# Performance work log

Hardware: AMD Instinct MI355X
Metric: run time of the kernel (lower is better)

Reference implementation:

```python
import jax, jax.numpy as jnp
import numpy as np

N_BLADES = 8
D_BLADE = 128
D_FFN = 512
LN_EPS = 1e-5


def _build_cayley_signs():
    """Cl(3,0) Cayley table: blades indexed by bitmask over {e1,e2,e3}.
    signs[i, j, k] = s where blade_i * blade_j = s * blade_k (Euclidean metric)."""
    def reorder_sign(a, b):
        a >>= 1
        total = 0
        while a:
            total += bin(a & b).count('1')
            a >>= 1
        return 1.0 if total % 2 == 0 else -1.0
    signs = np.zeros((8, 8, 8), dtype=np.float32)
    for i in range(8):
        for j in range(8):
            signs[i, j, i ^ j] = reorder_sign(i, j)
    return jnp.asarray(signs)


def setup_inputs() -> dict:
    key = jax.random.key(0)
    k_x, k_g, k_u, k_d = jax.random.split(key, 4)
    B, T = 4, 4096
    x = jax.random.normal(k_x, (B, T, N_BLADES, D_BLADE), dtype=jnp.float32)
    return {
        'x': x,
        'interaction_weights': jnp.full((N_BLADES, N_BLADES), 0.1, dtype=jnp.float32),
        'geo_gate': jnp.asarray(0.5, dtype=jnp.float32),
        'ln_w': jnp.ones((D_BLADE,), dtype=jnp.float32),
        'ln_b': jnp.zeros((D_BLADE,), dtype=jnp.float32),
        'w_gate': jax.random.normal(k_g, (D_FFN, D_BLADE), dtype=jnp.float32) * 0.02,
        'w_up': jax.random.normal(k_u, (D_FFN, D_BLADE), dtype=jnp.float32) * 0.02,
        'w_down': jax.random.normal(k_d, (D_BLADE, D_FFN), dtype=jnp.float32) * 0.02,
        'cayley_signs': _build_cayley_signs(),
    }


def reference(x, interaction_weights, geo_gate, ln_w, ln_b, w_gate, w_up, w_down, cayley_signs):
    # --- full geometric self-product via Cayley table ---
    w = jax.nn.sigmoid(interaction_weights)              # (i, j)
    signed = cayley_signs * w[:, :, None]                # (i, j, k): fold weights into sign tensor
    # result[b,t,k,d] = sum_ij signed[i,j,k] * x[b,t,i,d] * x[b,t,j,d]
    geo = jnp.einsum('btid,btjd,ijk->btkd', x, x, signed)
    # --- residual gate between geometric product and input ---
    gate = jax.nn.sigmoid(geo_gate)
    mixed = gate * geo + (1.0 - gate) * x                # (B, T, N, D)
    # --- per-blade LayerNorm over d_blade ---
    mu = jnp.mean(mixed, axis=-1, keepdims=True)
    var = jnp.mean(jnp.square(mixed - mu), axis=-1, keepdims=True)
    normed = (mixed - mu) * jax.lax.rsqrt(var + LN_EPS) * ln_w + ln_b
    # --- SwiGLU FFN (no biases) ---
    g = jnp.einsum('btnd,fd->btnf', normed, w_gate)
    u = jnp.einsum('btnd,fd->btnf', normed, w_up)
    h = jax.nn.silu(g) * u
    out = jnp.einsum('btnf,df->btnd', h, w_down)
    return x + out
```

## Files before the change

kernel.cpp:

```cpp
#include <hip/hip_runtime.h>
#include <hip/hip_bf16.h>

typedef unsigned short ushort_t;
typedef __bf16 bf16_t;
typedef bf16_t bf16x8 __attribute__((ext_vector_type(8)));
typedef unsigned short u16x8v __attribute__((ext_vector_type(8)));
typedef float f32x4 __attribute__((ext_vector_type(4)));
typedef unsigned uint32x2 __attribute__((ext_vector_type(2)));
typedef unsigned uint32x4 __attribute__((ext_vector_type(4)));

#define D 128
#define NB 8
#define DFFN 512
#define LN_EPS 1e-5f

#define BARRIER_LGKM() asm volatile("s_waitcnt lgkmcnt(0)\n\ts_barrier" ::: "memory")
#define BARRIER_VM()   asm volatile("s_waitcnt vmcnt(0) lgkmcnt(0)\n\ts_barrier" ::: "memory")

__device__ __forceinline__ ushort_t bf16_rne(float f) {
  union { float f; unsigned u; } c; c.f = f;
  unsigned u = c.u;
  unsigned r = (u + 0x7FFFu + ((u >> 16) & 1u)) >> 16;
  return (ushort_t)r;
}

__device__ __forceinline__ unsigned cvt_pk_bf16(float lo, float hi) {
  unsigned r;
  asm("v_cvt_pk_bf16_f32 %0, %1, %2" : "=v"(r) : "v"(lo), "v"(hi));
  return r;
}

__device__ __forceinline__ bf16x8 loadfrag_bf(const ushort_t* p) {
  u16x8v v = *(const u16x8v*)p;
  return __builtin_bit_cast(bf16x8, v);
}

__device__ __forceinline__ bf16x8 load8_cvt(const float* p) {
  f32x4 a = *(const f32x4*)p;
  f32x4 b = *(const f32x4*)(p + 4);
  u16x8v r;
  r[0] = bf16_rne(a[0]); r[1] = bf16_rne(a[1]);
  r[2] = bf16_rne(a[2]); r[3] = bf16_rne(a[3]);
  r[4] = bf16_rne(b[0]); r[5] = bf16_rne(b[1]);
  r[6] = bf16_rne(b[2]); r[7] = bf16_rne(b[3]);
  return __builtin_bit_cast(bf16x8, r);
}

__device__ __forceinline__ f32x4 mfma16(bf16x8 a, bf16x8 b, f32x4 c) {
  return __builtin_amdgcn_mfma_f32_16x16x32_bf16(a, b, c, 0, 0, 0);
}

__device__ __forceinline__ float readlane_f(float v, int lane) {
  return __builtin_bit_cast(float, __builtin_amdgcn_readlane(__builtin_bit_cast(int, v), lane));
}

__device__ __forceinline__ float fast_rcp(float x) {
  return __builtin_amdgcn_rcpf(x);
}

typedef const __attribute__((address_space(1))) void gv_t;
typedef __attribute__((address_space(3))) void lv_t;
__device__ __forceinline__ void gload_lds16(const void* g, void* l) {
  __builtin_amdgcn_global_load_lds((gv_t*)g, (lv_t*)l, 16, 0, 0);
}

__global__ void cvt_weights(const float* __restrict__ wg,
                            const float* __restrict__ wu,
                            const float* __restrict__ wd,
                            ushort_t* __restrict__ o) {
  int i = blockIdx.x * 256 + threadIdx.x;
  const int n1 = DFFN * D;
  float v;
  if (i < n1)            v = wg[i];
  else if (i < 2 * n1)   v = wu[i - n1];
  else                   v = wd[i - 2 * n1];
  o[i] = bf16_rne(v);
}

__global__ __launch_bounds__(256)
void geo_ln(const float* __restrict__ x,
            const float* __restrict__ iw,
            const float* __restrict__ geo_gate,
            const float* __restrict__ ln_w,
            const float* __restrict__ ln_b,
            const float* __restrict__ cayley,
            ushort_t* __restrict__ Aout) {
  const int tid = threadIdx.x;
  const int w = tid >> 6;
  const int l = tid & 63;
  const int g = l >> 4;
  const int q = l & 15;

  float sgv;
  {
    int i_l = l >> 3, j_l = l & 7;
    float s = cayley[(i_l * 8 + j_l) * 8 + (i_l ^ j_l)];
    sgv = s / (1.0f + __expf(-iw[i_l * 8 + j_l]));
  }
  float cd[8], cp[28];
#pragma unroll
  for (int i = 0; i < 8; ++i) cd[i] = readlane_f(sgv, i * 8 + i);
  {
    int p = 0;
#pragma unroll
    for (int i = 0; i < 8; ++i)
#pragma unroll
      for (int j = i + 1; j < 8; ++j) { cp[p] = readlane_f(sgv, i * 8 + j) + readlane_f(sgv, j * 8 + i); ++p; }
  }
  const float gate = 1.0f / (1.0f + __expf(-geo_gate[0]));
  const float ogate = 1.0f - gate;

  const f32x4 lw0 = *(const f32x4*)(ln_w + q * 8);
  const f32x4 lw1 = *(const f32x4*)(ln_w + q * 8 + 4);
  const f32x4 lb0 = *(const f32x4*)(ln_b + q * 8);
  const f32x4 lb1 = *(const f32x4*)(ln_b + q * 8 + 4);

  const long tok = (long)blockIdx.x * 16 + w * 4 + g;
  const float* xp = x + tok * (NB * D) + q * 8;

  f32x4 xa[8], xb[8];
#pragma unroll
  for (int i = 0; i < 8; ++i) { xa[i] = *(const f32x4*)(xp + i * D); xb[i] = *(const f32x4*)(xp + i * D + 4); }

  f32x4 ga[8], gb[8];
#pragma unroll
  for (int k = 0; k < 8; ++k) { ga[k] = 0.f; gb[k] = 0.f; }
#pragma unroll
  for (int i = 0; i < 8; ++i) {
    ga[0] += cd[i] * (xa[i] * xa[i]);
    gb[0] += cd[i] * (xb[i] * xb[i]);
  }
  {
    int p = 0;
#pragma unroll
    for (int i = 0; i < 8; ++i)
#pragma unroll
      for (int j = i + 1; j < 8; ++j) {
        int k = i ^ j;
        ga[k] += cp[p] * (xa[i] * xa[j]);
        gb[k] += cp[p] * (xb[i] * xb[j]);
        ++p;
      }
  }

  ushort_t* Arow0 = Aout + tok * (8 * D);
#pragma unroll
  for (int k = 0; k < 8; ++k) {
    f32x4 m0 = gate * ga[k] + ogate * xa[k];
    f32x4 m1 = gate * gb[k] + ogate * xb[k];
    float s1 = (m0[0] + m0[1]) + (m0[2] + m0[3]) + (m1[0] + m1[1]) + (m1[2] + m1[3]);
    float s2 = m0[0]*m0[0] + m0[1]*m0[1] + m0[2]*m0[2] + m0[3]*m0[3]
             + m1[0]*m1[0] + m1[1]*m1[1] + m1[2]*m1[2] + m1[3]*m1[3];
#pragma unroll
    for (int off = 8; off; off >>= 1) {
      s1 += __shfl_xor(s1, off, 64);
      s2 += __shfl_xor(s2, off, 64);
    }
    float mu = s1 * (1.0f / 128.0f);
    float rs = rsqrtf(s2 * (1.0f / 128.0f) - mu * mu + LN_EPS);
    float nb2 = -mu * rs;
    f32x4 n0, n1;
#pragma unroll
    for (int e = 0; e < 4; ++e) {
      n0[e] = (m0[e] * rs + nb2) * lw0[e] + lb0[e];
      n1[e] = (m1[e] * rs + nb2) * lw1[e] + lb1[e];
    }
    uint32x4 pk;
    pk[0] = cvt_pk_bf16(n0[0], n0[1]);
    pk[1] = cvt_pk_bf16(n0[2], n0[3]);
    pk[2] = cvt_pk_bf16(n1[0], n1[1]);
    pk[3] = cvt_pk_bf16(n1[2], n1[3]);
    *(uint32x4*)(Arow0 + k * D + ((q ^ k) * 8)) = pk;
  }
}

__global__ __launch_bounds__(256, 3)
void ffn_mfma(const ushort_t* __restrict__ Abf,
              const float* __restrict__ x,
              const ushort_t* __restrict__ wg_bf,
              const ushort_t* __restrict__ wu_bf,
              const ushort_t* __restrict__ wd_bf,
              float* __restrict__ out) {
  __shared__ ushort_t A[64 * 128];
  __shared__ ushort_t Hb[2][64 * 64];

  const int tid = threadIdx.x;
  const int w = tid >> 6;
  const int l = tid & 63;
  const int lg = l >> 4;
  const int ln16 = l & 15;

  const long row0 = (long)blockIdx.x * 64;

  {
    const ushort_t* src = Abf + row0 * D;
#pragma unroll
    for (int i = 0; i < 4; ++i) {
      int seg = w * 4 + i;
      gload_lds16(src + seg * 512 + l * 8, &A[seg * 512]);
    }
  }

  bf16x8 bg[4], bu[4], bd[2][2];
  {
    const int frow = w * 16 + ln16;
#pragma unroll
    for (int ks = 0; ks < 4; ++ks) {
      bg[ks] = loadfrag_bf(wg_bf + frow * D + ks * 32 + lg * 8);
      bu[ks] = loadfrag_bf(wu_bf + frow * D + ks * 32 + lg * 8);
    }
#pragma unroll
    for (int nt = 0; nt < 2; ++nt) {
      int dcol = w * 32 + nt * 16 + ln16;
#pragma unroll
      for (int k2 = 0; k2 < 2; ++k2)
        bd[nt][k2] = loadfrag_bf(wd_bf + dcol * DFFN + k2 * 32 + lg * 8);
    }
  }

  BARRIER_VM();

  f32x4 oacc[4][2];
#pragma unroll
  for (int mt = 0; mt < 4; ++mt)
#pragma unroll
    for (int nt = 0; nt < 2; ++nt)
#pragma unroll
      for (int r = 0; r < 4; ++r) oacc[mt][nt][r] = 0.f;

#pragma unroll
  for (int ch = 0; ch < 8; ++ch) {
    ushort_t* Hc = &Hb[ch & 1][0];

#pragma unroll
    for (int mt = 0; mt < 4; ++mt) {
      const int row = mt * 16 + ln16;
      f32x4 gacc = 0.f, uacc = 0.f;
      __builtin_amdgcn_s_setprio(1);
#pragma unroll
      for (int ks = 0; ks < 4; ++ks) {
        int unit = (ks * 4 + lg) ^ (row & 7);
        bf16x8 a = *(const bf16x8*)&A[row * 128 + unit * 8];
        gacc = mfma16(bg[ks], a, gacc);
        uacc = mfma16(bu[ks], a, uacc);
      }
      __builtin_amdgcn_s_setprio(0);
      float h[4];
#pragma unroll
      for (int r = 0; r < 4; ++r) {
        float gv = gacc[r];
        h[r] = gv * fast_rcp(1.0f + __expf(-gv)) * uacc[r];
      }
      uint32x2 pk;
      pk[0] = cvt_pk_bf16(h[0], h[1]);
      pk[1] = cvt_pk_bf16(h[2], h[3]);
      int u = (w * 2 + (lg >> 1)) ^ (row & 7);
      *(uint32x2*)((char*)Hc + row * 128 + u * 16 + (lg & 1) * 8) = pk;
    }

    if (ch < 7) {
      const int frow = (ch + 1) * 64 + w * 16 + ln16;
#pragma unroll
      for (int ks = 0; ks < 4; ++ks) {
        bg[ks] = loadfrag_bf(wg_bf + frow * D + ks * 32 + lg * 8);
        bu[ks] = loadfrag_bf(wu_bf + frow * D + ks * 32 + lg * 8);
      }
    }

    BARRIER_LGKM();

    __builtin_amdgcn_s_setprio(1);
#pragma unroll
    for (int mt = 0; mt < 4; ++mt) {
      const int m = mt * 16 + ln16;
#pragma unroll
      for (int k2 = 0; k2 < 2; ++k2) {
        int u = (k2 * 4 + lg) ^ (m & 7);
        bf16x8 hf = *(const bf16x8*)((const char*)Hc + m * 128 + u * 16);
        oacc[mt][0] = mfma16(hf, bd[0][k2], oacc[mt][0]);
        oacc[mt][1] = mfma16(hf, bd[1][k2], oacc[mt][1]);
      }
    }
    __builtin_amdgcn_s_setprio(0);

    if (ch < 7) {
#pragma unroll
      for (int nt = 0; nt < 2; ++nt) {
        int dcol = w * 32 + nt * 16 + ln16;
#pragma unroll
        for (int k2 = 0; k2 < 2; ++k2)
          bd[nt][k2] = loadfrag_bf(wd_bf + dcol * DFFN + (ch + 1) * 64 + k2 * 32 + lg * 8);
      }
    }
  }

#pragma unroll
  for (int mt = 0; mt < 4; ++mt) {
#pragma unroll
    for (int r = 0; r < 4; ++r) {
      long rowg = row0 + mt * 16 + lg * 4 + r;
      const float* xp = x + rowg * D;
      float* op = out + rowg * D;
#pragma unroll
      for (int nt = 0; nt < 2; ++nt) {
        int d = w * 32 + nt * 16 + ln16;
        op[d] = xp[d] + oacc[mt][nt][r];
      }
    }
  }
}

template <bool WS_BF16>
__global__ __launch_bounds__(256, 2)
void fused_geo_ffn(const float* __restrict__ x,
                   const float* __restrict__ iw,
                   const float* __restrict__ geo_gate,
                   const float* __restrict__ ln_w,
                   const float* __restrict__ ln_b,
                   const float* __restrict__ w_gate_f,
                   const float* __restrict__ w_up_f,
                   const float* __restrict__ w_down_f,
                   const float* __restrict__ cayley,
                   const ushort_t* __restrict__ wg_bf,
                   const ushort_t* __restrict__ wu_bf,
                   const ushort_t* __restrict__ wd_bf,
                   float* __restrict__ out) {
  __shared__ float sg[64];
  __shared__ ushort_t A_lds[128 * 128];
  __shared__ ushort_t H_lds[128 * 64];

  const int tid = threadIdx.x;
  const int w = tid >> 6;
  const int l = tid & 63;
  const int lg = l >> 4;
  const int ln16 = l & 15;
  const int kbase = lg * 8;

  if (tid < 64) {
    int i = tid >> 3, j = tid & 7;
    float s = cayley[(i * 8 + j) * 8 + (i ^ j)];
    sg[tid] = s / (1.0f + __expf(-iw[i * 8 + j]));
  }
  __syncthreads();
  float sgr[64];
#pragma unroll
  for (int t = 0; t < 64; ++t) sgr[t] = sg[t];

  const float gate = 1.0f / (1.0f + __expf(-geo_gate[0]));
  const float2 lw = *(const float2*)(ln_w + 2 * l);
  const float2 lb = *(const float2*)(ln_b + 2 * l);
  const long tok0 = (long)blockIdx.x * 16;

  for (int tt = 0; tt < 4; ++tt) {
    int ltok = w * 4 + tt;
    const float* xp = x + (tok0 + ltok) * (long)(NB * D);
    float2 xv[8];
#pragma unroll
    for (int i = 0; i < 8; ++i) xv[i] = *(const float2*)(xp + i * D + 2 * l);
#pragma unroll
    for (int k = 0; k < 8; ++k) {
      float2 g; g.x = 0.f; g.y = 0.f;
#pragma unroll
      for (int i = 0; i < 8; ++i) {
        float s = sgr[i * 8 + (i ^ k)];
        g.x += s * xv[i].x * xv[i ^ k].x;
        g.y += s * xv[i].y * xv[i ^ k].y;
      }
      float2 m;
      m.x = gate * g.x + (1.0f - gate) * xv[k].x;
      m.y = gate * g.y + (1.0f - gate) * xv[k].y;
      float s1 = m.x + m.y;
      float s2 = m.x * m.x + m.y * m.y;
#pragma unroll
      for (int off = 32; off; off >>= 1) {
        s1 += __shfl_xor(s1, off, 64);
        s2 += __shfl_xor(s2, off, 64);
      }
      float mu = s1 * (1.0f / 128.0f);
      float rs = rsqrtf(s2 * (1.0f / 128.0f) - mu * mu + LN_EPS);
      float nx = (m.x - mu) * rs * lw.x + lb.x;
      float ny = (m.y - mu) * rs * lw.y + lb.y;
      int row = ltok * 8 + k;
      int colb = (4 * l) ^ ((row & 7) << 4);
      *(unsigned*)((char*)A_lds + row * 256 + colb) = cvt_pk_bf16(nx, ny);
    }
  }
  __syncthreads();

  f32x4 oacc[8][2];
#pragma unroll
  for (int mt = 0; mt < 8; ++mt)
#pragma unroll
    for (int nt = 0; nt < 2; ++nt)
#pragma unroll
      for (int r = 0; r < 4; ++r) oacc[mt][nt][r] = 0.f;

  for (int ch = 0; ch < 8; ++ch) {
    const int fbase = ch * 64 + w * 16 + ln16;
    bf16x8 bg[4], bu[4];
#pragma unroll
    for (int ks = 0; ks < 4; ++ks) {
      int koff = ks * 32 + kbase;
      if (WS_BF16) {
        bg[ks] = loadfrag_bf(wg_bf + fbase * D + koff);
        bu[ks] = loadfrag_bf(wu_bf + fbase * D + koff);
      } else {
        bg[ks] = load8_cvt(w_gate_f + fbase * D + koff);
        bu[ks] = load8_cvt(w_up_f + fbase * D + koff);
      }
    }
#pragma unroll
    for (int mt = 0; mt < 8; ++mt) {
      const int row = mt * 16 + ln16;
      f32x4 gacc = 0.f, uacc = 0.f;
#pragma unroll
      for (int ks = 0; ks < 4; ++ks) {
        int colb = ((ks * 32 + kbase) * 2) ^ ((row & 7) << 4);
        bf16x8 a = *(const bf16x8*)((const char*)A_lds + row * 256 + colb);
        gacc = mfma16(bg[ks], a, gacc);
        uacc = mfma16(bu[ks], a, uacc);
      }
      float h[4];
#pragma unroll
      for (int r = 0; r < 4; ++r) {
        float gv = gacc[r], uv = uacc[r];
        h[r] = gv * __builtin_amdgcn_rcpf(1.0f + __expf(-gv)) * uv;
      }
      uint32x2 pk;
      pk[0] = cvt_pk_bf16(h[0], h[1]);
      pk[1] = cvt_pk_bf16(h[2], h[3]);
      int u = (w * 2 + (lg >> 1)) ^ (row & 7);
      *(uint32x2*)&H_lds[row * 64 + u * 8 + (lg & 1) * 4] = pk;
    }
    __syncthreads();
#pragma unroll
    for (int mt = 0; mt < 8; ++mt) {
      const int row = mt * 16 + ln16;
#pragma unroll
      for (int ks = 0; ks < 2; ++ks) {
        int u = (ks * 4 + lg) ^ (row & 7);
        bf16x8 hfrag = *(const bf16x8*)&H_lds[row * 64 + u * 8];
        bf16x8 b0, b1;
        int dcol0 = w * 32 + ln16;
        int foff = ch * 64 + ks * 32 + kbase;
        if (WS_BF16) {
          b0 = loadfrag_bf(wd_bf + dcol0 * DFFN + foff);
          b1 = loadfrag_bf(wd_bf + (dcol0 + 16) * DFFN + foff);
        } else {
          b0 = load8_cvt(w_down_f + dcol0 * DFFN + foff);
          b1 = load8_cvt(w_down_f + (dcol0 + 16) * DFFN + foff);
        }
        oacc[mt][0] = mfma16(hfrag, b0, oacc[mt][0]);
        oacc[mt][1] = mfma16(hfrag, b1, oacc[mt][1]);
      }
    }
    __syncthreads();
  }

  const long rowg0 = tok0 * NB;
#pragma unroll
  for (int mt = 0; mt < 8; ++mt) {
#pragma unroll
    for (int r = 0; r < 4; ++r) {
      long row = rowg0 + mt * 16 + lg * 4 + r;
      const float* xp = x + row * D;
      float* op = out + row * D;
#pragma unroll
      for (int nt = 0; nt < 2; ++nt) {
        int d = w * 32 + nt * 16 + ln16;
        op[d] = xp[d] + oacc[mt][nt][r];
      }
    }
  }
}

extern "C" void kernel_launch(void* const* d_in, const int* in_sizes, int n_in,
                              void* d_out, int out_size, void* d_ws, size_t ws_size,
                              hipStream_t stream) {
  const float* x   = (const float*)d_in[0];
  const float* iw  = (const float*)d_in[1];
  const float* gg  = (const float*)d_in[2];
  const float* lnw = (const float*)d_in[3];
  const float* lnb = (const float*)d_in[4];
  const float* wg  = (const float*)d_in[5];
  const float* wu  = (const float*)d_in[6];
  const float* wd  = (const float*)d_in[7];
  const float* cs  = (const float*)d_in[8];
  float* out = (float*)d_out;

  const int ntok = in_sizes[0] / (NB * D);
  const int wtot = 3 * DFFN * D;
  const size_t wbytes = (size_t)wtot * 2;
  const size_t abytes = (size_t)ntok * NB * D * 2;

  if (ws_size >= wbytes + abytes) {
    ushort_t* wbf = (ushort_t*)d_ws;
    ushort_t* act = wbf + wtot;
    cvt_weights<<<wtot / 256, 256, 0, stream>>>(wg, wu, wd, wbf);
    geo_ln<<<ntok / 16, 256, 0, stream>>>(x, iw, gg, lnw, lnb, cs, act);
    ffn_mfma<<<(ntok * NB) / 64, 256, 0, stream>>>(
        act, x, wbf, wbf + DFFN * D, wbf + 2 * DFFN * D, out);
  } else if (ws_size >= wbytes) {
    ushort_t* wbf = (ushort_t*)d_ws;
    cvt_weights<<<wtot / 256, 256, 0, stream>>>(wg, wu, wd, wbf);
    fused_geo_ffn<true><<<ntok / 16, 256, 0, stream>>>(
        x, iw, gg, lnw, lnb, wg, wu, wd, cs,
        wbf, wbf + DFFN * D, wbf + 2 * DFFN * D, out);
  } else {
    fused_geo_ffn<false><<<ntok / 16, 256, 0, stream>>>(
        x, iw, gg, lnw, lnb, wg, wu, wd, cs,
        (const ushort_t*)nullptr, (const ushort_t*)nullptr, (const ushort_t*)nullptr, out);
  }
}
```

Before: 123.4 us.

## Software-pipeline gate/up GEMM of next chunk with down-proj of current chunk

```diff
diff --git a/kernel.cpp b/kernel.cpp
--- a/kernel.cpp
+++ b/kernel.cpp
@@ -174,7 +174,7 @@
   }
 }
 
-__global__ __launch_bounds__(256, 3)
+__global__ __launch_bounds__(256, 4)
 void ffn_mfma(const ushort_t* __restrict__ Abf,
               const float* __restrict__ x,
               const ushort_t* __restrict__ wg_bf,
@@ -202,23 +202,56 @@
   }
 
   bf16x8 bg[4], bu[4], bd[2][2];
+  const int frow_base = w * 16 + ln16;
+  const int dcol0 = w * 32 + ln16;
+  const int dcol1 = w * 32 + 16 + ln16;
   {
-    const int frow = w * 16 + ln16;
+#pragma unroll
+    for (int ks = 0; ks < 4; ++ks) {
+      bg[ks] = loadfrag_bf(wg_bf + frow_base * D + ks * 32 + lg * 8);
+      bu[ks] = loadfrag_bf(wu_bf + frow_base * D + ks * 32 + lg * 8);
+    }
+#pragma unroll
+    for (int k2 = 0; k2 < 2; ++k2) {
+      bd[0][k2] = loadfrag_bf(wd_bf + dcol0 * DFFN + k2 * 32 + lg * 8);
+      bd[1][k2] = loadfrag_bf(wd_bf + dcol1 * DFFN + k2 * 32 + lg * 8);
+    }
+  }
+
+  BARRIER_VM();
+
+#pragma unroll
+  for (int mt = 0; mt < 4; ++mt) {
+    const int row = mt * 16 + ln16;
+    f32x4 gacc = 0.f, uacc = 0.f;
+#pragma unroll
+    for (int ks = 0; ks < 4; ++ks) {
+      int unit = (ks * 4 + lg) ^ (row & 7);
+      bf16x8 a = *(const bf16x8*)&A[row * 128 + unit * 8];
+      gacc = mfma16(bg[ks], a, gacc);
+      uacc = mfma16(bu[ks], a, uacc);
+    }
+    float h[4];
+#pragma unroll
+    for (int r = 0; r < 4; ++r) {
+      float gv = gacc[r];
+      h[r] = gv * fast_rcp(1.0f + __expf(-gv)) * uacc[r];
+    }
+    uint32x2 pk;
+    pk[0] = cvt_pk_bf16(h[0], h[1]);
+    pk[1] = cvt_pk_bf16(h[2], h[3]);
+    int u = (w * 2 + (lg >> 1)) ^ (row & 7);
+    *(uint32x2*)((char*)&Hb[0][0] + row * 128 + u * 16 + (lg & 1) * 8) = pk;
+  }
+
+  {
+    const int frow = 64 + frow_base;
 #pragma unroll
     for (int ks = 0; ks < 4; ++ks) {
       bg[ks] = loadfrag_bf(wg_bf + frow * D + ks * 32 + lg * 8);
       bu[ks] = loadfrag_bf(wu_bf + frow * D + ks * 32 + lg * 8);
     }
-#pragma unroll
-    for (int nt = 0; nt < 2; ++nt) {
-      int dcol = w * 32 + nt * 16 + ln16;
-#pragma unroll
-      for (int k2 = 0; k2 < 2; ++k2)
-        bd[nt][k2] = loadfrag_bf(wd_bf + dcol * DFFN + k2 * 32 + lg * 8);
-    }
-  }
-
-  BARRIER_VM();
+  }
 
   f32x4 oacc[4][2];
 #pragma unroll
@@ -231,41 +264,7 @@
 #pragma unroll
   for (int ch = 0; ch < 8; ++ch) {
     ushort_t* Hc = &Hb[ch & 1][0];
-
-#pragma unroll
-    for (int mt = 0; mt < 4; ++mt) {
-      const int row = mt * 16 + ln16;
-      f32x4 gacc = 0.f, uacc = 0.f;
-      __builtin_amdgcn_s_setprio(1);
-#pragma unroll
-      for (int ks = 0; ks < 4; ++ks) {
-        int unit = (ks * 4 + lg) ^ (row & 7);
-        bf16x8 a = *(const bf16x8*)&A[row * 128 + unit * 8];
-        gacc = mfma16(bg[ks], a, gacc);
-        uacc = mfma16(bu[ks], a, uacc);
-      }
-      __builtin_amdgcn_s_setprio(0);
-      float h[4];
-#pragma unroll
-      for (int r = 0; r < 4; ++r) {
-        float gv = gacc[r];
-        h[r] = gv * fast_rcp(1.0f + __expf(-gv)) * uacc[r];
-      }
-      uint32x2 pk;
-      pk[0] = cvt_pk_bf16(h[0], h[1]);
-      pk[1] = cvt_pk_bf16(h[2], h[3]);
-      int u = (w * 2 + (lg >> 1)) ^ (row & 7);
-      *(uint32x2*)((char*)Hc + row * 128 + u * 16 + (lg & 1) * 8) = pk;
-    }
-
-    if (ch < 7) {
-      const int frow = (ch + 1) * 64 + w * 16 + ln16;
-#pragma unroll
-      for (int ks = 0; ks < 4; ++ks) {
-        bg[ks] = loadfrag_bf(wg_bf + frow * D + ks * 32 + lg * 8);
-        bu[ks] = loadfrag_bf(wu_bf + frow * D + ks * 32 + lg * 8);
-      }
-    }
+    ushort_t* Hn = &Hb[(ch + 1) & 1][0];
 
     BARRIER_LGKM();
 
@@ -273,6 +272,7 @@
 #pragma unroll
     for (int mt = 0; mt < 4; ++mt) {
       const int m = mt * 16 + ln16;
+
 #pragma unroll
       for (int k2 = 0; k2 < 2; ++k2) {
         int u = (k2 * 4 + lg) ^ (m & 7);
@@ -280,16 +280,44 @@
         oacc[mt][0] = mfma16(hf, bd[0][k2], oacc[mt][0]);
         oacc[mt][1] = mfma16(hf, bd[1][k2], oacc[mt][1]);
       }
+
+      if (ch < 7) {
+        f32x4 gacc = 0.f, uacc = 0.f;
+#pragma unroll
+        for (int ks = 0; ks < 4; ++ks) {
+          int unit = (ks * 4 + lg) ^ (m & 7);
+          bf16x8 a = *(const bf16x8*)&A[m * 128 + unit * 8];
+          gacc = mfma16(bg[ks], a, gacc);
+          uacc = mfma16(bu[ks], a, uacc);
+        }
+        float h[4];
+#pragma unroll
+        for (int r = 0; r < 4; ++r) {
+          float gv = gacc[r];
+          h[r] = gv * fast_rcp(1.0f + __expf(-gv)) * uacc[r];
+        }
+        uint32x2 pk;
+        pk[0] = cvt_pk_bf16(h[0], h[1]);
+        pk[1] = cvt_pk_bf16(h[2], h[3]);
+        int u = (w * 2 + (lg >> 1)) ^ (m & 7);
+        *(uint32x2*)((char*)Hn + m * 128 + u * 16 + (lg & 1) * 8) = pk;
+      }
     }
     __builtin_amdgcn_s_setprio(0);
 
     if (ch < 7) {
 #pragma unroll
-      for (int nt = 0; nt < 2; ++nt) {
-        int dcol = w * 32 + nt * 16 + ln16;
-#pragma unroll
-        for (int k2 = 0; k2 < 2; ++k2)
-          bd[nt][k2] = loadfrag_bf(wd_bf + dcol * DFFN + (ch + 1) * 64 + k2 * 32 + lg * 8);
+      for (int k2 = 0; k2 < 2; ++k2) {
+        bd[0][k2] = loadfrag_bf(wd_bf + dcol0 * DFFN + (ch + 1) * 64 + k2 * 32 + lg * 8);
+        bd[1][k2] = loadfrag_bf(wd_bf + dcol1 * DFFN + (ch + 1) * 64 + k2 * 32 + lg * 8);
+      }
+      if (ch < 6) {
+        const int frow = (ch + 2) * 64 + frow_base;
+#pragma unroll
+        for (int ks = 0; ks < 4; ++ks) {
+          bg[ks] = loadfrag_bf(wg_bf + frow * D + ks * 32 + lg * 8);
+          bu[ks] = loadfrag_bf(wu_bf + frow * D + ks * 32 + lg * 8);
+        }
       }
     }
   }
```

New measurement: 148.0 us. 20.0% more time.

## Keep A and H fragments in registers and split FFN over waves by rows and features

Applied to the files above, without the earlier changes.

```diff
diff --git a/kernel.cpp b/kernel.cpp
--- a/kernel.cpp
+++ b/kernel.cpp
@@ -5,6 +5,7 @@
 typedef __bf16 bf16_t;
 typedef bf16_t bf16x8 __attribute__((ext_vector_type(8)));
 typedef unsigned short u16x8v __attribute__((ext_vector_type(8)));
+typedef unsigned short u16x4 __attribute__((ext_vector_type(4)));
 typedef float f32x4 __attribute__((ext_vector_type(4)));
 typedef unsigned uint32x2 __attribute__((ext_vector_type(2)));
 typedef unsigned uint32x4 __attribute__((ext_vector_type(4)));
@@ -13,6 +14,7 @@
 #define NB 8
 #define DFFN 512
 #define LN_EPS 1e-5f
+#define REDSTRIDE 129
 
 #define BARRIER_LGKM() asm volatile("s_waitcnt lgkmcnt(0)\n\ts_barrier" ::: "memory")
 #define BARRIER_VM()   asm volatile("s_waitcnt vmcnt(0) lgkmcnt(0)\n\ts_barrier" ::: "memory")
@@ -174,21 +176,24 @@
   }
 }
 
-__global__ __launch_bounds__(256, 3)
-void ffn_mfma(const ushort_t* __restrict__ Abf,
-              const float* __restrict__ x,
-              const ushort_t* __restrict__ wg_bf,
-              const ushort_t* __restrict__ wu_bf,
-              const ushort_t* __restrict__ wd_bf,
-              float* __restrict__ out) {
-  __shared__ ushort_t A[64 * 128];
-  __shared__ ushort_t Hb[2][64 * 64];
+__global__ __launch_bounds__(256, 2)
+void ffn_v2(const ushort_t* __restrict__ Abf,
+            const float* __restrict__ x,
+            const ushort_t* __restrict__ wg_bf,
+            const ushort_t* __restrict__ wu_bf,
+            const ushort_t* __restrict__ wd_bf,
+            float* __restrict__ out) {
+  __shared__ char SMEM[2 * 32 * REDSTRIDE * 4];
+  ushort_t* A = (ushort_t*)SMEM;
+  float* red = (float*)SMEM;
 
   const int tid = threadIdx.x;
   const int w = tid >> 6;
   const int l = tid & 63;
   const int lg = l >> 4;
   const int ln16 = l & 15;
+  const int mh = w & 1;
+  const int fh = w >> 1;
 
   const long row0 = (long)blockIdx.x * 64;
 
@@ -200,111 +205,125 @@
       gload_lds16(src + seg * 512 + l * 8, &A[seg * 512]);
     }
   }
-
-  bf16x8 bg[4], bu[4], bd[2][2];
-  {
-    const int frow = w * 16 + ln16;
+  BARRIER_VM();
+
+  bf16x8 afr[2][4];
+#pragma unroll
+  for (int mt = 0; mt < 2; ++mt) {
+    const int row = mh * 32 + mt * 16 + ln16;
 #pragma unroll
     for (int ks = 0; ks < 4; ++ks) {
-      bg[ks] = loadfrag_bf(wg_bf + frow * D + ks * 32 + lg * 8);
-      bu[ks] = loadfrag_bf(wu_bf + frow * D + ks * 32 + lg * 8);
-    }
-#pragma unroll
-    for (int nt = 0; nt < 2; ++nt) {
-      int dcol = w * 32 + nt * 16 + ln16;
-#pragma unroll
-      for (int k2 = 0; k2 < 2; ++k2)
-        bd[nt][k2] = loadfrag_bf(wd_bf + dcol * DFFN + k2 * 32 + lg * 8);
-    }
-  }
-
-  BARRIER_VM();
-
-  f32x4 oacc[4][2];
-#pragma unroll
-  for (int mt = 0; mt < 4; ++mt)
-#pragma unroll
-    for (int nt = 0; nt < 2; ++nt)
+      int unit = (ks * 4 + lg) ^ (row & 7);
+      afr[mt][ks] = *(const bf16x8*)&A[row * 128 + unit * 8];
+    }
+  }
+  BARRIER_LGKM();
+
+  f32x4 oacc[2][8];
+#pragma unroll
+  for (int mt = 0; mt < 2; ++mt)
+#pragma unroll
+    for (int nt = 0; nt < 8; ++nt)
 #pragma unroll
       for (int r = 0; r < 4; ++r) oacc[mt][nt][r] = 0.f;
 
 #pragma unroll
   for (int ch = 0; ch < 8; ++ch) {
-    ushort_t* Hc = &Hb[ch & 1][0];
-
-#pragma unroll
-    for (int mt = 0; mt < 4; ++mt) {
-      const int row = mt * 16 + ln16;
-      f32x4 gacc = 0.f, uacc = 0.f;
-      __builtin_amdgcn_s_setprio(1);
+    const int fb = ch * 64 + fh * 32;
+
+    bf16x8 bg[2][4], bu[2][4];
+#pragma unroll
+    for (int s = 0; s < 2; ++s) {
+      const int frow = fb + s * 16 + ln16;
 #pragma unroll
       for (int ks = 0; ks < 4; ++ks) {
-        int unit = (ks * 4 + lg) ^ (row & 7);
-        bf16x8 a = *(const bf16x8*)&A[row * 128 + unit * 8];
-        gacc = mfma16(bg[ks], a, gacc);
-        uacc = mfma16(bu[ks], a, uacc);
-      }
-      __builtin_amdgcn_s_setprio(0);
-      float h[4];
+        bg[s][ks] = loadfrag_bf(wg_bf + frow * D + ks * 32 + lg * 8);
+        bu[s][ks] = loadfrag_bf(wu_bf + frow * D + ks * 32 + lg * 8);
+      }
+    }
+    bf16x8 bd[8];
+#pragma unroll
+    for (int nt = 0; nt < 8; ++nt) {
+      const ushort_t* wp = wd_bf + (nt * 16 + ln16) * DFFN + fb + lg * 4;
+      u16x4 lo = *(const u16x4*)wp;
+      u16x4 hi = *(const u16x4*)(wp + 16);
+      u16x8v v = __builtin_shufflevector(lo, hi, 0, 1, 2, 3, 4, 5, 6, 7);
+      bd[nt] = __builtin_bit_cast(bf16x8, v);
+    }
+
+    f32x4 gacc[2][2], uacc[2][2];
+#pragma unroll
+    for (int s = 0; s < 2; ++s)
+#pragma unroll
+      for (int mt = 0; mt < 2; ++mt) { gacc[s][mt] = 0.f; uacc[s][mt] = 0.f; }
+    __builtin_amdgcn_s_setprio(1);
+#pragma unroll
+    for (int s = 0; s < 2; ++s)
+#pragma unroll
+      for (int mt = 0; mt < 2; ++mt)
+#pragma unroll
+        for (int ks = 0; ks < 4; ++ks) {
+          gacc[s][mt] = mfma16(bg[s][ks], afr[mt][ks], gacc[s][mt]);
+          uacc[s][mt] = mfma16(bu[s][ks], afr[mt][ks], uacc[s][mt]);
+        }
+    __builtin_amdgcn_s_setprio(0);
+
+    bf16x8 a2[2];
+#pragma unroll
+    for (int mt = 0; mt < 2; ++mt) {
+      float h0[4], h1[4];
 #pragma unroll
       for (int r = 0; r < 4; ++r) {
-        float gv = gacc[r];
-        h[r] = gv * fast_rcp(1.0f + __expf(-gv)) * uacc[r];
-      }
-      uint32x2 pk;
-      pk[0] = cvt_pk_bf16(h[0], h[1]);
-      pk[1] = cvt_pk_bf16(h[2], h[3]);
-      int u = (w * 2 + (lg >> 1)) ^ (row & 7);
-      *(uint32x2*)((char*)Hc + row * 128 + u * 16 + (lg & 1) * 8) = pk;
-    }
-
-    if (ch < 7) {
-      const int frow = (ch + 1) * 64 + w * 16 + ln16;
-#pragma unroll
-      for (int ks = 0; ks < 4; ++ks) {
-        bg[ks] = loadfrag_bf(wg_bf + frow * D + ks * 32 + lg * 8);
-        bu[ks] = loadfrag_bf(wu_bf + frow * D + ks * 32 + lg * 8);
-      }
-    }
-
-    BARRIER_LGKM();
+        float g0 = gacc[0][mt][r];
+        h0[r] = g0 * fast_rcp(1.0f + __expf(-g0)) * uacc[0][mt][r];
+        float g1 = gacc[1][mt][r];
+        h1[r] = g1 * fast_rcp(1.0f + __expf(-g1)) * uacc[1][mt][r];
+      }
+      uint32x4 pk;
+      pk[0] = cvt_pk_bf16(h0[0], h0[1]);
+      pk[1] = cvt_pk_bf16(h0[2], h0[3]);
+      pk[2] = cvt_pk_bf16(h1[0], h1[1]);
+      pk[3] = cvt_pk_bf16(h1[2], h1[3]);
+      a2[mt] = __builtin_bit_cast(bf16x8, pk);
+    }
 
     __builtin_amdgcn_s_setprio(1);
 #pragma unroll
-    for (int mt = 0; mt < 4; ++mt) {
-      const int m = mt * 16 + ln16;
-#pragma unroll
-      for (int k2 = 0; k2 < 2; ++k2) {
-        int u = (k2 * 4 + lg) ^ (m & 7);
-        bf16x8 hf = *(const bf16x8*)((const char*)Hc + m * 128 + u * 16);
-        oacc[mt][0] = mfma16(hf, bd[0][k2], oacc[mt][0]);
-        oacc[mt][1] = mfma16(hf, bd[1][k2], oacc[mt][1]);
-      }
-    }
+    for (int mt = 0; mt < 2; ++mt)
+#pragma unroll
+      for (int nt = 0; nt < 8; ++nt)
+        oacc[mt][nt] = mfma16(a2[mt], bd[nt], oacc[mt][nt]);
     __builtin_amdgcn_s_setprio(0);
-
-    if (ch < 7) {
-#pragma unroll
-      for (int nt = 0; nt < 2; ++nt) {
-        int dcol = w * 32 + nt * 16 + ln16;
-#pragma unroll
-        for (int k2 = 0; k2 < 2; ++k2)
-          bd[nt][k2] = loadfrag_bf(wd_bf + dcol * DFFN + (ch + 1) * 64 + k2 * 32 + lg * 8);
-      }
-    }
-  }
-
-#pragma unroll
-  for (int mt = 0; mt < 4; ++mt) {
-#pragma unroll
-    for (int r = 0; r < 4; ++r) {
-      long rowg = row0 + mt * 16 + lg * 4 + r;
-      const float* xp = x + rowg * D;
-      float* op = out + rowg * D;
-#pragma unroll
-      for (int nt = 0; nt < 2; ++nt) {
-        int d = w * 32 + nt * 16 + ln16;
-        op[d] = xp[d] + oacc[mt][nt][r];
+  }
+
+  if (fh == 1) {
+    float* rp = red + mh * 32 * REDSTRIDE;
+#pragma unroll
+    for (int mt = 0; mt < 2; ++mt)
+#pragma unroll
+      for (int r = 0; r < 4; ++r) {
+        const int rrow = mt * 16 + lg * 4 + r;
+#pragma unroll
+        for (int nt = 0; nt < 8; ++nt)
+          rp[rrow * REDSTRIDE + nt * 16 + ln16] = oacc[mt][nt][r];
+      }
+  }
+  BARRIER_LGKM();
+  if (fh == 0) {
+    const float* rp = red + mh * 32 * REDSTRIDE;
+#pragma unroll
+    for (int mt = 0; mt < 2; ++mt) {
+#pragma unroll
+      for (int r = 0; r < 4; ++r) {
+        const int rrow = mt * 16 + lg * 4 + r;
+        const long rowg = row0 + mh * 32 + rrow;
+        const float* xp = x + rowg * D;
+        float* op = out + rowg * D;
+#pragma unroll
+        for (int nt = 0; nt < 8; ++nt) {
+          int d = nt * 16 + ln16;
+          op[d] = xp[d] + oacc[mt][nt][r] + rp[rrow * REDSTRIDE + d];
+        }
       }
     }
   }
@@ -498,7 +517,7 @@
     ushort_t* act = wbf + wtot;
     cvt_weights<<<wtot / 256, 256, 0, stream>>>(wg, wu, wd, wbf);
     geo_ln<<<ntok / 16, 256, 0, stream>>>(x, iw, gg, lnw, lnb, cs, act);
-    ffn_mfma<<<(ntok * NB) / 64, 256, 0, stream>>>(
+    ffn_v2<<<(ntok * NB) / 64, 256, 0, stream>>>(
         act, x, wbf, wbf + DFFN * D, wbf + 2 * DFFN * D, out);
   } else if (ws_size >= wbytes) {
     ushort_t* wbf = (ushort_t*)d_ws;
```

Measured after the change: 260.9 us. 2.11x slower.
